# Kernel tuning notes

Measured on AMD Instinct MI355X. Metric: run time of the kernel, lower is better.

The kernel has to match this reference:

```python
import jax, jax.numpy as jnp
import numpy as np

N_NODES, N_EDGES = 50000, 800000
IN_DIM, HID, HEADS, OUT_DIM = 256, 32, 8, 16
NEG_SLOPE = 0.2  # PyG GATConv default leaky-relu slope
EPS = 1e-16      # PyG softmax denominator epsilon


def setup_inputs() -> dict:
    key = jax.random.key(0)
    ks = jax.random.split(key, 12)
    x = jax.random.normal(ks[0], (N_NODES, IN_DIM), dtype=jnp.float32)
    edge_index = jax.random.randint(ks[1], (2, N_EDGES), 0, N_NODES, dtype=jnp.int32)
    s1 = 1.0 / np.sqrt(IN_DIM)
    s2 = 1.0 / np.sqrt(HID * HEADS)
    return {
        "x": x,
        "edge_index": edge_index,
        "W1": jax.random.normal(ks[2], (IN_DIM, HEADS * HID), dtype=jnp.float32) * s1,
        "att_src1": jax.random.normal(ks[3], (HEADS, HID), dtype=jnp.float32) * s1,
        "att_dst1": jax.random.normal(ks[4], (HEADS, HID), dtype=jnp.float32) * s1,
        "bias1": jnp.zeros((HEADS * HID,), dtype=jnp.float32),
        "W2": jax.random.normal(ks[5], (HEADS * HID, HEADS * OUT_DIM), dtype=jnp.float32) * s2,
        "att_src2": jax.random.normal(ks[6], (HEADS, OUT_DIM), dtype=jnp.float32) * s2,
        "att_dst2": jax.random.normal(ks[7], (HEADS, OUT_DIM), dtype=jnp.float32) * s2,
        "bias2": jnp.zeros((OUT_DIM,), dtype=jnp.float32),
    }


def _gat_conv(x, src, dst, W, att_src, att_dst, bias, concat):
    # x: [N, F_in]; src/dst: [E'] (self-loops already appended)
    N = x.shape[0]
    H, C = att_src.shape
    h = (x @ W).reshape(N, H, C)                      # [N, H, C]
    a_src = jnp.einsum('nhc,hc->nh', h, att_src)      # [N, H]
    a_dst = jnp.einsum('nhc,hc->nh', h, att_dst)
    e = a_src[src] + a_dst[dst]                       # [E', H]
    e = jax.nn.leaky_relu(e, NEG_SLOPE)
    # segment softmax over edges grouped by destination node
    m = jax.ops.segment_max(e, dst, num_segments=N)   # [N, H]
    e = jnp.exp(e - m[dst])
    denom = jax.ops.segment_sum(e, dst, num_segments=N)
    alpha = e / (denom[dst] + EPS)                    # [E', H]
    msg = h[src] * alpha[:, :, None]                  # [E', H, C] gather+weight
    out = jax.ops.segment_sum(msg, dst, num_segments=N)  # [N, H, C] scatter-add
    if concat:
        out = out.reshape(N, H * C)
    else:
        out = out.mean(axis=1)
    return out + bias


def reference(x, edge_index, W1, att_src1, att_dst1, bias1, W2, att_src2, att_dst2, bias2):
    N = x.shape[0]
    loop = jnp.arange(N, dtype=edge_index.dtype)
    src = jnp.concatenate([edge_index[0], loop])  # PyG add_self_loops=True
    dst = jnp.concatenate([edge_index[1], loop])
    h = _gat_conv(x, src, dst, W1, att_src1, att_dst1, bias1, concat=True)
    h = jax.nn.elu(h)
    out = _gat_conv(h, src, dst, W2, att_src2, att_dst2, bias2, concat=False)
    return out
```

## Files before the change

kernel.cpp:

```cpp
#include <hip/hip_runtime.h>

#define N_NODES 50000
#define N_EDGES 800000
#define EP (N_EDGES + N_NODES)
#define HEADS 8
#define NEG 0.2f

typedef __attribute__((ext_vector_type(8))) short bf16x8;
typedef __attribute__((ext_vector_type(8))) unsigned short u16x8;
typedef __attribute__((ext_vector_type(4))) float f32x4;


__device__ __forceinline__ float bf2f(unsigned short u) {
    return __uint_as_float(((unsigned)u) << 16);
}
__device__ __forceinline__ unsigned short f2bf(float f) {
    unsigned u = __float_as_uint(f);
    return (unsigned short)((u + 0x7FFFu + ((u >> 16) & 1u)) >> 16);
}

__device__ __forceinline__ void get_edge(const int* __restrict__ ei, int e, int& s, int& d) {
    if (e < N_EDGES) { s = ei[e]; d = ei[N_EDGES + e]; }
    else             { s = d = e - N_EDGES; }
}

__device__ __forceinline__ float lrelu(float v) { return v > 0.f ? v : NEG * v; }


#define PREP_X4 3200000
__global__ void prep_kernel(const float* __restrict__ x, const float* __restrict__ W1,
                            const float* __restrict__ W2, unsigned short* __restrict__ xb,
                            unsigned short* __restrict__ W1T, unsigned short* __restrict__ W2T) {
    int t = blockIdx.x * 256 + threadIdx.x;
    if (t < PREP_X4) {
        float4 v = ((const float4*)x)[t];
        ushort4 o;
        o.x = f2bf(v.x); o.y = f2bf(v.y); o.z = f2bf(v.z); o.w = f2bf(v.w);
        ((ushort4*)xb)[t] = o;
    } else if (t < PREP_X4 + 65536) {
        int u = t - PREP_X4; int k = u >> 8, n = u & 255;
        W1T[n * 256 + k] = f2bf(W1[k * 256 + n]);
    } else if (t < PREP_X4 + 65536 + 32768) {
        int u = t - (PREP_X4 + 65536); int k = u >> 7, n = u & 127;
        W2T[n * 256 + k] = f2bf(W2[k * 128 + n]);
    }
}


__global__ void hist_kernel(const int* __restrict__ ei, int* __restrict__ cnt) {
    int e = blockIdx.x * 256 + threadIdx.x;
    if (e >= EP) return;
    int s, d; get_edge(ei, e, s, d);
    atomicAdd(&cnt[d], 1);
}

#define SCAN_BLOCKS 196

__global__ __launch_bounds__(256) void scan_p1(const int* __restrict__ cnt,
                                               int* __restrict__ incl, int* __restrict__ bsum) {
    __shared__ int wsum[4];
    const int tid = threadIdx.x, lane = tid & 63, wid = tid >> 6;
    const int idx = blockIdx.x * 256 + tid;
    int v = (idx < N_NODES) ? cnt[idx] : 0;
#pragma unroll
    for (int off = 1; off < 64; off <<= 1) {
        int t = __shfl_up(v, off);
        if (lane >= off) v += t;
    }
    if (lane == 63) wsum[wid] = v;
    __syncthreads();
    int add = 0;
#pragma unroll
    for (int w = 0; w < 4; w++) add += (w < wid) ? wsum[w] : 0;
    incl[idx] = v + add;
    if (tid == 255) bsum[blockIdx.x] = v + add;
}

__global__ __launch_bounds__(256) void scan_p2(const int* __restrict__ bsum,
                                               int* __restrict__ bex) {
    __shared__ int wsum[4];
    const int tid = threadIdx.x, lane = tid & 63, wid = tid >> 6;
    int v0 = (tid < SCAN_BLOCKS) ? bsum[tid] : 0;
    int v = v0;
#pragma unroll
    for (int off = 1; off < 64; off <<= 1) {
        int t = __shfl_up(v, off);
        if (lane >= off) v += t;
    }
    if (lane == 63) wsum[wid] = v;
    __syncthreads();
    int add = 0;
#pragma unroll
    for (int w = 0; w < 4; w++) add += (w < wid) ? wsum[w] : 0;
    if (tid < SCAN_BLOCKS) bex[tid] = v + add - v0;
}

__global__ __launch_bounds__(256) void scan_p3(const int* __restrict__ incl,
                                               const int* __restrict__ bex,
                                               int* __restrict__ cnt_cursor,
                                               int* __restrict__ row_start) {
    const int idx = blockIdx.x * 256 + threadIdx.x;
    if (idx == 0) row_start[N_NODES] = EP;
    if (idx >= N_NODES) return;
    int ex = bex[blockIdx.x] + incl[idx] - cnt_cursor[idx];
    row_start[idx] = ex;
    cnt_cursor[idx] = ex;
}

__global__ void fill_kernel(const int* __restrict__ ei, int* __restrict__ cursor,
                            unsigned short* __restrict__ csr) {
    int e = blockIdx.x * 256 + threadIdx.x;
    if (e >= EP) return;
    int s, d; get_edge(ei, e, s, d);
    int pos = atomicAdd(&cursor[d], 1);
    csr[pos] = (unsigned short)s;
}


template<int NC, int C>
__global__ __launch_bounds__(256) void gemm_fused(const unsigned short* __restrict__ A,
        const unsigned short* __restrict__ WT,
        const float* __restrict__ att_s, const float* __restrict__ att_d,
        unsigned short* __restrict__ outh,
        float* __restrict__ a_src, float* __restrict__ a_dst) {
    constexpr int WN  = NC / 4;
    constexpr int NT  = WN / 16;
    constexpr int TPH = C / 16;
    constexpr int BJ  = NC / 32;
    __shared__ unsigned short As[64 * 64];
    __shared__ unsigned short Bs[NC * 64];
    const int m0 = blockIdx.x * 64;
    const int tid  = threadIdx.x;
    const int wave = tid >> 6, lane = tid & 63;
    const int col = lane & 15, quad = lane >> 4;
    const int ar = tid >> 2;
    const int ac = tid & 3;

    f32x4 acc[4][NT] = {};

    for (int k0 = 0; k0 < 256; k0 += 64) {
        u16x8 av[2];
#pragma unroll
        for (int j = 0; j < 2; j++)
            av[j] = *(const u16x8*)(A + (size_t)(m0 + ar) * 256 + k0 + (ac + j * 4) * 8);
        u16x8 bv[BJ];
#pragma unroll
        for (int j = 0; j < BJ; j++) {
            int idx = j * 256 + tid, row = idx >> 3, ch = idx & 7;
            bv[j] = *(const u16x8*)(WT + (size_t)row * 256 + k0 + ch * 8);
        }
        __syncthreads();
#pragma unroll
        for (int j = 0; j < 2; j++) {
            int ch = ac + j * 4;
            *(u16x8*)&As[ar * 64 + (ch ^ (ar & 7)) * 8] = av[j];
        }
#pragma unroll
        for (int j = 0; j < BJ; j++) {
            int idx = j * 256 + tid, row = idx >> 3, ch = idx & 7;
            *(u16x8*)&Bs[row * 64 + (ch ^ (row & 7)) * 8] = bv[j];
        }
        __syncthreads();
#pragma unroll
        for (int ks = 0; ks < 64; ks += 32) {
            bf16x8 af[4], bfm[NT];
#pragma unroll
            for (int mi = 0; mi < 4; mi++) {
                int r = mi * 16 + col, c = (ks >> 3) + quad;
                af[mi] = *(const bf16x8*)&As[r * 64 + (c ^ (r & 7)) * 8];
            }
#pragma unroll
            for (int ni = 0; ni < NT; ni++) {
                int r = wave * WN + ni * 16 + col, c = (ks >> 3) + quad;
                bfm[ni] = *(const bf16x8*)&Bs[r * 64 + (c ^ (r & 7)) * 8];
            }
#pragma unroll
            for (int mi = 0; mi < 4; mi++)
#pragma unroll
                for (int ni = 0; ni < NT; ni++)
                    acc[mi][ni] = __builtin_amdgcn_mfma_f32_16x16x32_bf16(
                        af[mi], bfm[ni], acc[mi][ni], 0, 0, 0);
        }
    }

#pragma unroll
    for (int mi = 0; mi < 4; mi++)
#pragma unroll
        for (int ni = 0; ni < NT; ni++)
#pragma unroll
            for (int r = 0; r < 4; r++) {
                int m = m0 + mi * 16 + quad * 4 + r;
                if (m < N_NODES)
                    outh[(size_t)m * NC + wave * WN + ni * 16 + col] = f2bf(acc[mi][ni][r]);
            }

    float asv[NT], adv[NT];
#pragma unroll
    for (int ni = 0; ni < NT; ni++) {
        int n = wave * WN + ni * 16 + col;
        asv[ni] = att_s[n];
        adv[ni] = att_d[n];
    }
#pragma unroll
    for (int mi = 0; mi < 4; mi++)
#pragma unroll
        for (int r = 0; r < 4; r++) {
#pragma unroll
            for (int hl = 0; hl < 2; hl++) {
                float s = 0.f, d = 0.f;
#pragma unroll
                for (int t = 0; t < TPH; t++) {
                    int ni = hl * TPH + t;
                    s = fmaf(acc[mi][ni][r], asv[ni], s);
                    d = fmaf(acc[mi][ni][r], adv[ni], d);
                }
#pragma unroll
                for (int off = 1; off < 16; off <<= 1) {
                    s += __shfl_xor(s, off);
                    d += __shfl_xor(d, off);
                }
                if (col == 0) {
                    int m = m0 + mi * 16 + quad * 4 + r;
                    if (m < N_NODES) {
                        int hh = wave * 2 + hl;
                        a_src[m * 8 + hh] = s;
                        a_dst[m * 8 + hh] = d;
                    }
                }
            }
        }
}


template<int C, bool LAYER2>
__global__ __launch_bounds__(256) void gat_agg_fused(const int* __restrict__ row_start,
        const unsigned short* __restrict__ csr,
        const unsigned short* __restrict__ hfeat, const float* __restrict__ a_src,
        const float* __restrict__ a_dst, const float* __restrict__ bias,
        void* __restrict__ outp) {
    constexpr int F  = 8 * C;
    constexpr int VF = F / 64;
    const int n    = blockIdx.x * 4 + (threadIdx.x >> 6);
    const int lane = threadIdx.x & 63;
    if (n >= N_NODES) return;

    const int rs  = row_start[n];
    const int deg = row_start[n + 1] - rs;
    const int hf  = lane >> 3;
    const float adstf = a_dst[n * 8 + hf];

    float acc[VF] = {};
    float den = 0.f;

    for (int c0 = 0; c0 < deg; c0 += 64) {
        const int cnt = min(64, deg - c0);
        int myid = (lane < cnt) ? (int)csr[rs + c0 + lane] : 0;
        int e = 0;
        for (; e + 8 <= cnt; e += 8) {
            int ss[8];
#pragma unroll
            for (int j = 0; j < 8; j++) ss[j] = __shfl(myid, e + j);
            float as[8];
#pragma unroll
            for (int j = 0; j < 8; j++) as[j] = a_src[ss[j] * 8 + hf];
            if constexpr (!LAYER2) {
                ushort4 v[8];
#pragma unroll
                for (int j = 0; j < 8; j++)
                    v[j] = *(const ushort4*)(hfeat + (size_t)ss[j] * F + lane * 4);
#pragma unroll
                for (int j = 0; j < 8; j++) {
                    float w = __expf(lrelu(as[j] + adstf));
                    den += w;
                    acc[0] = fmaf(w, bf2f(v[j].x), acc[0]);
                    acc[1] = fmaf(w, bf2f(v[j].y), acc[1]);
                    acc[2] = fmaf(w, bf2f(v[j].z), acc[2]);
                    acc[3] = fmaf(w, bf2f(v[j].w), acc[3]);
                }
            } else {
                ushort2 v[8];
#pragma unroll
                for (int j = 0; j < 8; j++)
                    v[j] = *(const ushort2*)(hfeat + (size_t)ss[j] * F + lane * 2);
#pragma unroll
                for (int j = 0; j < 8; j++) {
                    float w = __expf(lrelu(as[j] + adstf));
                    den += w;
                    acc[0] = fmaf(w, bf2f(v[j].x), acc[0]);
                    acc[1] = fmaf(w, bf2f(v[j].y), acc[1]);
                }
            }
        }
        for (; e < cnt; e++) {
            int s = __shfl(myid, e);
            float w = __expf(lrelu(a_src[s * 8 + hf] + adstf));
            den += w;
            if constexpr (!LAYER2) {
                ushort4 hv = *(const ushort4*)(hfeat + (size_t)s * F + lane * 4);
                acc[0] = fmaf(w, bf2f(hv.x), acc[0]); acc[1] = fmaf(w, bf2f(hv.y), acc[1]);
                acc[2] = fmaf(w, bf2f(hv.z), acc[2]); acc[3] = fmaf(w, bf2f(hv.w), acc[3]);
            } else {
                ushort2 hv = *(const ushort2*)(hfeat + (size_t)s * F + lane * 2);
                acc[0] = fmaf(w, bf2f(hv.x), acc[0]); acc[1] = fmaf(w, bf2f(hv.y), acc[1]);
            }
        }
    }

    const float inv = 1.f / (den + 1e-16f);

    if constexpr (!LAYER2) {
        ushort4 o;
        float v0 = acc[0] * inv + bias[lane * 4 + 0];
        float v1 = acc[1] * inv + bias[lane * 4 + 1];
        float v2 = acc[2] * inv + bias[lane * 4 + 2];
        float v3 = acc[3] * inv + bias[lane * 4 + 3];
        o.x = f2bf(v0 > 0.f ? v0 : __expf(v0) - 1.f);
        o.y = f2bf(v1 > 0.f ? v1 : __expf(v1) - 1.f);
        o.z = f2bf(v2 > 0.f ? v2 : __expf(v2) - 1.f);
        o.w = f2bf(v3 > 0.f ? v3 : __expf(v3) - 1.f);
        *(ushort4*)((unsigned short*)outp + (size_t)n * F + lane * 4) = o;
    } else {
        float a0 = acc[0] * inv, a1 = acc[1] * inv;
#pragma unroll
        for (int off = 8; off <= 32; off <<= 1) {
            a0 += __shfl_xor(a0, off);
            a1 += __shfl_xor(a1, off);
        }
        if (lane < 8) {
            float2 o;
            o.x = a0 * 0.125f + bias[lane * 2 + 0];
            o.y = a1 * 0.125f + bias[lane * 2 + 1];
            *(float2*)((float*)outp + (size_t)n * 16 + lane * 2) = o;
        }
    }
}


extern "C" void kernel_launch(void* const* d_in, const int* in_sizes, int n_in,
                              void* d_out, int out_size, void* d_ws, size_t ws_size,
                              hipStream_t stream) {
    const float* x        = (const float*)d_in[0];
    const int*   ei       = (const int*)d_in[1];
    const float* W1       = (const float*)d_in[2];
    const float* att_src1 = (const float*)d_in[3];
    const float* att_dst1 = (const float*)d_in[4];
    const float* bias1    = (const float*)d_in[5];
    const float* W2       = (const float*)d_in[6];
    const float* att_src2 = (const float*)d_in[7];
    const float* att_dst2 = (const float*)d_in[8];
    const float* bias2    = (const float*)d_in[9];
    float* out = (float*)d_out;

    char* ws = (char*)d_ws;
    unsigned short* h1  = (unsigned short*)(ws);
    unsigned short* h2  = (unsigned short*)(ws);
    unsigned short* xb  = (unsigned short*)(ws + 32ull * 1024 * 1024);
    unsigned short* x2b = (unsigned short*)(ws + 64ull * 1024 * 1024);
    unsigned short* W1T = (unsigned short*)(ws + 96ull * 1024 * 1024);
    unsigned short* W2T = W1T + 65536;
    char* aux = ws + 97ull * 1024 * 1024;
    float*          a_src     = (float*)(aux);
    float*          a_dst     = (float*)(aux + 1600000);
    int*            row_start = (int*)  (aux + 3200000);
    int*            cnt       = (int*)  (aux + 3400064);
    unsigned short* csr       = (unsigned short*)(aux + 3600128);
    int*            incl      = (int*)  (aux + 5300128);
    int*            bsum      = (int*)  (aux + 5500832);
    int*            bex       = (int*)  (aux + 5501632);

    const int E_BLOCKS  = (EP + 255) / 256;
    const int MT = (N_NODES + 63) / 64;
    const int AGG_BLOCKS = (N_NODES + 3) / 4;
    const int PREP_BLOCKS = (PREP_X4 + 65536 + 32768 + 255) / 256;

    hipMemsetAsync(cnt, 0, N_NODES * sizeof(int), stream);
    prep_kernel<<<PREP_BLOCKS, 256, 0, stream>>>(x, W1, W2, xb, W1T, W2T);
    hist_kernel<<<E_BLOCKS, 256, 0, stream>>>(ei, cnt);
    scan_p1<<<SCAN_BLOCKS, 256, 0, stream>>>(cnt, incl, bsum);
    scan_p2<<<1, 256, 0, stream>>>(bsum, bex);
    scan_p3<<<SCAN_BLOCKS, 256, 0, stream>>>(incl, bex, cnt, row_start);
    fill_kernel<<<E_BLOCKS, 256, 0, stream>>>(ei, cnt, csr);

    gemm_fused<256, 32><<<MT, 256, 0, stream>>>(xb, W1T, att_src1, att_dst1, h1, a_src, a_dst);
    gat_agg_fused<32, false><<<AGG_BLOCKS, 256, 0, stream>>>(row_start, csr, h1, a_src, a_dst, bias1, x2b);

    gemm_fused<128, 16><<<MT, 256, 0, stream>>>(x2b, W2T, att_src2, att_dst2, h2, a_src, a_dst);
    gat_agg_fused<16, true><<<AGG_BLOCKS, 256, 0, stream>>>(row_start, csr, h2, a_src, a_dst, bias2, out);
}
```

Baseline: 350.7 us.

## Fuse x bf16 conversion into GEMM, merge weight prep with histogram, widen L1 gather

The layer-1 GEMM now reads fp32 x directly and converts it to bf16 in registers, which removes the separate conversion pass and the xb buffer round trip (about 51MB read plus 25MB write). The weight transpose/convert is folded into the histogram kernel launch. The layer-1 aggregation is rewritten so each half-wave handles a different edge with 16-byte feature loads, processing two edges per step, and the halves are combined at the end. The GEMM now does twice the A-load bytes per thread and clamps out-of-range rows.

```diff
diff --git a/kernel.cpp b/kernel.cpp
--- a/kernel.cpp
+++ b/kernel.cpp
@@ -27,32 +27,31 @@
 __device__ __forceinline__ float lrelu(float v) { return v > 0.f ? v : NEG * v; }
 
 
-#define PREP_X4 3200000
-__global__ void prep_kernel(const float* __restrict__ x, const float* __restrict__ W1,
-                            const float* __restrict__ W2, unsigned short* __restrict__ xb,
-                            unsigned short* __restrict__ W1T, unsigned short* __restrict__ W2T) {
-    int t = blockIdx.x * 256 + threadIdx.x;
-    if (t < PREP_X4) {
-        float4 v = ((const float4*)x)[t];
-        ushort4 o;
-        o.x = f2bf(v.x); o.y = f2bf(v.y); o.z = f2bf(v.z); o.w = f2bf(v.w);
-        ((ushort4*)xb)[t] = o;
-    } else if (t < PREP_X4 + 65536) {
-        int u = t - PREP_X4; int k = u >> 8, n = u & 255;
-        W1T[n * 256 + k] = f2bf(W1[k * 256 + n]);
-    } else if (t < PREP_X4 + 65536 + 32768) {
-        int u = t - (PREP_X4 + 65536); int k = u >> 7, n = u & 127;
-        W2T[n * 256 + k] = f2bf(W2[k * 128 + n]);
-    }
-}
-
-
-__global__ void hist_kernel(const int* __restrict__ ei, int* __restrict__ cnt) {
-    int e = blockIdx.x * 256 + threadIdx.x;
-    if (e >= EP) return;
-    int s, d; get_edge(ei, e, s, d);
-    atomicAdd(&cnt[d], 1);
-}
+#define E_BLOCKS ((EP + 255) / 256)
+#define W_ITEMS  (65536 + 32768)
+#define W_BLOCKS ((W_ITEMS + 255) / 256)
+
+__global__ void hist_prep(const int* __restrict__ ei, int* __restrict__ cnt,
+                          const float* __restrict__ W1, const float* __restrict__ W2,
+                          unsigned short* __restrict__ W1T, unsigned short* __restrict__ W2T) {
+    const int b = blockIdx.x;
+    if (b < E_BLOCKS) {
+        int e = b * 256 + threadIdx.x;
+        if (e >= EP) return;
+        int s, d; get_edge(ei, e, s, d);
+        atomicAdd(&cnt[d], 1);
+    } else {
+        int t = (b - E_BLOCKS) * 256 + threadIdx.x;
+        if (t < 65536) {
+            int k = t >> 8, n = t & 255;
+            W1T[n * 256 + k] = f2bf(W1[k * 256 + n]);
+        } else if (t < W_ITEMS) {
+            int u = t - 65536; int k = u >> 7, n = u & 127;
+            W2T[n * 256 + k] = f2bf(W2[k * 128 + n]);
+        }
+    }
+}
+
 
 #define SCAN_BLOCKS 196
 
@@ -117,8 +116,8 @@
 }
 
 
-template<int NC, int C>
-__global__ __launch_bounds__(256) void gemm_fused(const unsigned short* __restrict__ A,
+template<int NC, int C, bool AF32>
+__global__ __launch_bounds__(256) void gemm_fused(const void* __restrict__ Aptr,
         const unsigned short* __restrict__ WT,
         const float* __restrict__ att_s, const float* __restrict__ att_d,
         unsigned short* __restrict__ outh,
@@ -135,14 +134,30 @@
     const int col = lane & 15, quad = lane >> 4;
     const int ar = tid >> 2;
     const int ac = tid & 3;
+    const int arow = min(m0 + ar, N_NODES - 1);
 
     f32x4 acc[4][NT] = {};
 
     for (int k0 = 0; k0 < 256; k0 += 64) {
         u16x8 av[2];
-#pragma unroll
-        for (int j = 0; j < 2; j++)
-            av[j] = *(const u16x8*)(A + (size_t)(m0 + ar) * 256 + k0 + (ac + j * 4) * 8);
+        if constexpr (AF32) {
+            const float* Af = (const float*)Aptr;
+#pragma unroll
+            for (int j = 0; j < 2; j++) {
+                const float* p = Af + (size_t)arow * 256 + k0 + (ac + j * 4) * 8;
+                float4 f0 = *(const float4*)p;
+                float4 f1 = *(const float4*)(p + 4);
+                u16x8 v;
+                v[0] = f2bf(f0.x); v[1] = f2bf(f0.y); v[2] = f2bf(f0.z); v[3] = f2bf(f0.w);
+                v[4] = f2bf(f1.x); v[5] = f2bf(f1.y); v[6] = f2bf(f1.z); v[7] = f2bf(f1.w);
+                av[j] = v;
+            }
+        } else {
+            const unsigned short* Ab = (const unsigned short*)Aptr;
+#pragma unroll
+            for (int j = 0; j < 2; j++)
+                av[j] = *(const u16x8*)(Ab + (size_t)arow * 256 + k0 + (ac + j * 4) * 8);
+        }
         u16x8 bv[BJ];
 #pragma unroll
         for (int j = 0; j < BJ; j++) {
@@ -232,14 +247,87 @@
 }
 
 
-template<int C, bool LAYER2>
-__global__ __launch_bounds__(256) void gat_agg_fused(const int* __restrict__ row_start,
+__global__ __launch_bounds__(256) void gat_agg_l1(const int* __restrict__ row_start,
         const unsigned short* __restrict__ csr,
         const unsigned short* __restrict__ hfeat, const float* __restrict__ a_src,
         const float* __restrict__ a_dst, const float* __restrict__ bias,
-        void* __restrict__ outp) {
-    constexpr int F  = 8 * C;
-    constexpr int VF = F / 64;
+        unsigned short* __restrict__ outp) {
+    const int n    = blockIdx.x * 4 + (threadIdx.x >> 6);
+    const int lane = threadIdx.x & 63;
+    if (n >= N_NODES) return;
+
+    const int rs  = row_start[n];
+    const int deg = row_start[n + 1] - rs;
+    const int p   = lane >> 5;
+    const int q   = lane & 31;
+    const int hq  = q >> 2;
+    const float adstf = a_dst[n * 8 + hq];
+
+    float acc[8] = {};
+    float den = 0.f;
+
+    for (int c0 = 0; c0 < deg; c0 += 64) {
+        const int cnt = min(64, deg - c0);
+        int myid = (lane < cnt) ? (int)csr[rs + c0 + lane] : 0;
+        int e = 0;
+        for (; e + 8 <= cnt; e += 8) {
+            int ss[4];
+#pragma unroll
+            for (int j = 0; j < 4; j++) ss[j] = __shfl(myid, e + j * 2 + p);
+            float as[4];
+#pragma unroll
+            for (int j = 0; j < 4; j++) as[j] = a_src[ss[j] * 8 + hq];
+            u16x8 v[4];
+#pragma unroll
+            for (int j = 0; j < 4; j++)
+                v[j] = *(const u16x8*)(hfeat + (size_t)ss[j] * 256 + q * 8);
+#pragma unroll
+            for (int j = 0; j < 4; j++) {
+                float w = __expf(lrelu(as[j] + adstf));
+                den += w;
+#pragma unroll
+                for (int k = 0; k < 8; k++)
+                    acc[k] = fmaf(w, bf2f(v[j][k]), acc[k]);
+            }
+        }
+        for (; e < cnt; e += 2) {
+            int idx = e + p;
+            bool ok = idx < cnt;
+            int s = __shfl(myid, ok ? idx : cnt - 1);
+            float w = ok ? __expf(lrelu(a_src[s * 8 + hq] + adstf)) : 0.f;
+            den += w;
+            u16x8 v = *(const u16x8*)(hfeat + (size_t)s * 256 + q * 8);
+#pragma unroll
+            for (int k = 0; k < 8; k++)
+                acc[k] = fmaf(w, bf2f(v[k]), acc[k]);
+        }
+    }
+
+    den += __shfl_xor(den, 32);
+#pragma unroll
+    for (int k = 0; k < 8; k++) acc[k] += __shfl_xor(acc[k], 32);
+
+    if (p == 0) {
+        const float inv = 1.f / (den + 1e-16f);
+        float4 b0 = *(const float4*)(bias + q * 8);
+        float4 b1 = *(const float4*)(bias + q * 8 + 4);
+        float bb[8] = {b0.x, b0.y, b0.z, b0.w, b1.x, b1.y, b1.z, b1.w};
+        u16x8 o;
+#pragma unroll
+        for (int k = 0; k < 8; k++) {
+            float v = acc[k] * inv + bb[k];
+            o[k] = f2bf(v > 0.f ? v : __expf(v) - 1.f);
+        }
+        *(u16x8*)(outp + (size_t)n * 256 + q * 8) = o;
+    }
+}
+
+
+__global__ __launch_bounds__(256) void gat_agg_l2(const int* __restrict__ row_start,
+        const unsigned short* __restrict__ csr,
+        const unsigned short* __restrict__ hfeat, const float* __restrict__ a_src,
+        const float* __restrict__ a_dst, const float* __restrict__ bias,
+        float* __restrict__ outp) {
     const int n    = blockIdx.x * 4 + (threadIdx.x >> 6);
     const int lane = threadIdx.x & 63;
     if (n >= N_NODES) return;
@@ -249,8 +337,7 @@
     const int hf  = lane >> 3;
     const float adstf = a_dst[n * 8 + hf];
 
-    float acc[VF] = {};
-    float den = 0.f;
+    float acc0 = 0.f, acc1 = 0.f, den = 0.f;
 
     for (int c0 = 0; c0 < deg; c0 += 64) {
         const int cnt = min(64, deg - c0);
@@ -263,75 +350,40 @@
             float as[8];
 #pragma unroll
             for (int j = 0; j < 8; j++) as[j] = a_src[ss[j] * 8 + hf];
-            if constexpr (!LAYER2) {
-                ushort4 v[8];
-#pragma unroll
-                for (int j = 0; j < 8; j++)
-                    v[j] = *(const ushort4*)(hfeat + (size_t)ss[j] * F + lane * 4);
-#pragma unroll
-                for (int j = 0; j < 8; j++) {
-                    float w = __expf(lrelu(as[j] + adstf));
-                    den += w;
-                    acc[0] = fmaf(w, bf2f(v[j].x), acc[0]);
-                    acc[1] = fmaf(w, bf2f(v[j].y), acc[1]);
-                    acc[2] = fmaf(w, bf2f(v[j].z), acc[2]);
-                    acc[3] = fmaf(w, bf2f(v[j].w), acc[3]);
-                }
-            } else {
-                ushort2 v[8];
-#pragma unroll
-                for (int j = 0; j < 8; j++)
-                    v[j] = *(const ushort2*)(hfeat + (size_t)ss[j] * F + lane * 2);
-#pragma unroll
-                for (int j = 0; j < 8; j++) {
-                    float w = __expf(lrelu(as[j] + adstf));
-                    den += w;
-                    acc[0] = fmaf(w, bf2f(v[j].x), acc[0]);
-                    acc[1] = fmaf(w, bf2f(v[j].y), acc[1]);
-                }
+            ushort2 v[8];
+#pragma unroll
+            for (int j = 0; j < 8; j++)
+                v[j] = *(const ushort2*)(hfeat + (size_t)ss[j] * 128 + lane * 2);
+#pragma unroll
+            for (int j = 0; j < 8; j++) {
+                float w = __expf(lrelu(as[j] + adstf));
+                den += w;
+                acc0 = fmaf(w, bf2f(v[j].x), acc0);
+                acc1 = fmaf(w, bf2f(v[j].y), acc1);
             }
         }
         for (; e < cnt; e++) {
             int s = __shfl(myid, e);
             float w = __expf(lrelu(a_src[s * 8 + hf] + adstf));
             den += w;
-            if constexpr (!LAYER2) {
-                ushort4 hv = *(const ushort4*)(hfeat + (size_t)s * F + lane * 4);
-                acc[0] = fmaf(w, bf2f(hv.x), acc[0]); acc[1] = fmaf(w, bf2f(hv.y), acc[1]);
-                acc[2] = fmaf(w, bf2f(hv.z), acc[2]); acc[3] = fmaf(w, bf2f(hv.w), acc[3]);
-            } else {
-                ushort2 hv = *(const ushort2*)(hfeat + (size_t)s * F + lane * 2);
-                acc[0] = fmaf(w, bf2f(hv.x), acc[0]); acc[1] = fmaf(w, bf2f(hv.y), acc[1]);
-            }
+            ushort2 hv = *(const ushort2*)(hfeat + (size_t)s * 128 + lane * 2);
+            acc0 = fmaf(w, bf2f(hv.x), acc0);
+            acc1 = fmaf(w, bf2f(hv.y), acc1);
         }
     }
 
     const float inv = 1.f / (den + 1e-16f);
-
-    if constexpr (!LAYER2) {
-        ushort4 o;
-        float v0 = acc[0] * inv + bias[lane * 4 + 0];
-        float v1 = acc[1] * inv + bias[lane * 4 + 1];
-        float v2 = acc[2] * inv + bias[lane * 4 + 2];
-        float v3 = acc[3] * inv + bias[lane * 4 + 3];
-        o.x = f2bf(v0 > 0.f ? v0 : __expf(v0) - 1.f);
-        o.y = f2bf(v1 > 0.f ? v1 : __expf(v1) - 1.f);
-        o.z = f2bf(v2 > 0.f ? v2 : __expf(v2) - 1.f);
-        o.w = f2bf(v3 > 0.f ? v3 : __expf(v3) - 1.f);
-        *(ushort4*)((unsigned short*)outp + (size_t)n * F + lane * 4) = o;
-    } else {
-        float a0 = acc[0] * inv, a1 = acc[1] * inv;
-#pragma unroll
-        for (int off = 8; off <= 32; off <<= 1) {
-            a0 += __shfl_xor(a0, off);
-            a1 += __shfl_xor(a1, off);
-        }
-        if (lane < 8) {
-            float2 o;
-            o.x = a0 * 0.125f + bias[lane * 2 + 0];
-            o.y = a1 * 0.125f + bias[lane * 2 + 1];
-            *(float2*)((float*)outp + (size_t)n * 16 + lane * 2) = o;
-        }
+    float a0 = acc0 * inv, a1 = acc1 * inv;
+#pragma unroll
+    for (int off = 8; off <= 32; off <<= 1) {
+        a0 += __shfl_xor(a0, off);
+        a1 += __shfl_xor(a1, off);
+    }
+    if (lane < 8) {
+        float2 o;
+        o.x = a0 * 0.125f + bias[lane * 2 + 0];
+        o.y = a1 * 0.125f + bias[lane * 2 + 1];
+        *(float2*)(outp + (size_t)n * 16 + lane * 2) = o;
     }
 }
 
@@ -354,11 +406,10 @@
     char* ws = (char*)d_ws;
     unsigned short* h1  = (unsigned short*)(ws);
     unsigned short* h2  = (unsigned short*)(ws);
-    unsigned short* xb  = (unsigned short*)(ws + 32ull * 1024 * 1024);
-    unsigned short* x2b = (unsigned short*)(ws + 64ull * 1024 * 1024);
-    unsigned short* W1T = (unsigned short*)(ws + 96ull * 1024 * 1024);
+    unsigned short* x2b = (unsigned short*)(ws + 32ull * 1024 * 1024);
+    unsigned short* W1T = (unsigned short*)(ws + 64ull * 1024 * 1024);
     unsigned short* W2T = W1T + 65536;
-    char* aux = ws + 97ull * 1024 * 1024;
+    char* aux = ws + 66ull * 1024 * 1024;
     float*          a_src     = (float*)(aux);
     float*          a_dst     = (float*)(aux + 1600000);
     int*            row_start = (int*)  (aux + 3200000);
@@ -368,22 +419,19 @@
     int*            bsum      = (int*)  (aux + 5500832);
     int*            bex       = (int*)  (aux + 5501632);
 
-    const int E_BLOCKS  = (EP + 255) / 256;
     const int MT = (N_NODES + 63) / 64;
     const int AGG_BLOCKS = (N_NODES + 3) / 4;
-    const int PREP_BLOCKS = (PREP_X4 + 65536 + 32768 + 255) / 256;
 
     hipMemsetAsync(cnt, 0, N_NODES * sizeof(int), stream);
-    prep_kernel<<<PREP_BLOCKS, 256, 0, stream>>>(x, W1, W2, xb, W1T, W2T);
-    hist_kernel<<<E_BLOCKS, 256, 0, stream>>>(ei, cnt);
+    hist_prep<<<E_BLOCKS + W_BLOCKS, 256, 0, stream>>>(ei, cnt, W1, W2, W1T, W2T);
     scan_p1<<<SCAN_BLOCKS, 256, 0, stream>>>(cnt, incl, bsum);
     scan_p2<<<1, 256, 0, stream>>>(bsum, bex);
     scan_p3<<<SCAN_BLOCKS, 256, 0, stream>>>(incl, bex, cnt, row_start);
     fill_kernel<<<E_BLOCKS, 256, 0, stream>>>(ei, cnt, csr);
 
-    gemm_fused<256, 32><<<MT, 256, 0, stream>>>(xb, W1T, att_src1, att_dst1, h1, a_src, a_dst);
-    gat_agg_fused<32, false><<<AGG_BLOCKS, 256, 0, stream>>>(row_start, csr, h1, a_src, a_dst, bias1, x2b);
-
-    gemm_fused<128, 16><<<MT, 256, 0, stream>>>(x2b, W2T, att_src2, att_dst2, h2, a_src, a_dst);
-    gat_agg_fused<16, true><<<AGG_BLOCKS, 256, 0, stream>>>(row_start, csr, h2, a_src, a_dst, bias2, out);
-}
+    gemm_fused<256, 32, true><<<MT, 256, 0, stream>>>(x, W1T, att_src1, att_dst1, h1, a_src, a_dst);
+    gat_agg_l1<<<AGG_BLOCKS, 256, 0, stream>>>(row_start, csr, h1, a_src, a_dst, bias1, x2b);
+
+    gemm_fused<128, 16, false><<<MT, 256, 0, stream>>>(x2b, W2T, att_src2, att_dst2, h2, a_src, a_dst);
+    gat_agg_l2<<<AGG_BLOCKS, 256, 0, stream>>>(row_start, csr, h2, a_src, a_dst, bias2, out);
+}
```

After: 341.7 us. 1.03x faster.
